# Kernel optimization log

Hardware: AMD Instinct MI355X
Metric: run time of the kernel (lower is better)

## Reference

```python
import jax, jax.numpy as jnp
import numpy as np

B, T, C, H = 2, 2048, 1024, 16
HD = C // H  # head dim = 64


def setup_inputs() -> dict:
    key = jax.random.key(0)
    k0, k1, k2 = jax.random.split(key, 3)
    x = jax.random.normal(k0, (B, T, C), jnp.float32)
    W_attn = jax.random.normal(k1, (C, 3 * C), jnp.float32) * 0.02
    b_attn = jnp.zeros((3 * C,), jnp.float32)
    W_proj = jax.random.normal(k2, (C, C), jnp.float32) * 0.02
    b_proj = jnp.zeros((C,), jnp.float32)
    # rope: (1,1,T,HD//2,2,2) stack of 2x2 rotation matrices [[cos,-sin],[sin,cos]]
    inv_freq = 1.0 / (10000.0 ** (jnp.arange(0, HD, 2, dtype=jnp.float32) / HD))
    ang = jnp.arange(T, dtype=jnp.float32)[:, None] * inv_freq[None, :]  # (T, HD//2)
    cos, sin = jnp.cos(ang), jnp.sin(ang)
    rope = jnp.stack([jnp.stack([cos, -sin], -1), jnp.stack([sin, cos], -1)], -2)
    rope = rope[None, None]  # (1,1,T,HD//2,2,2)
    return dict(x=x, W_attn=W_attn, b_attn=b_attn, W_proj=W_proj, b_proj=b_proj, rope=rope)


def reference(x, W_attn, b_attn, W_proj, b_proj, rope):
    Bv, Tv, Cv = x.shape
    Hd = Cv // H
    qkv = x @ W_attn + b_attn                      # (B,T,3C) fused QKV proj
    q, k, v = jnp.split(qkv, 3, axis=-1)

    def heads(t):
        return t.reshape(Bv, Tv, H, Hd).transpose(0, 2, 1, 3)  # (B,H,T,Hd)

    q, k, v = heads(q), heads(k), heads(v)

    cos = rope[..., 0, 0][..., None]               # (1,1,T,Hd//2,1)
    sin = rope[..., 1, 0][..., None]

    def rot(t):
        tr = t.reshape(Bv, H, Tv, Hd // 2, 2)
        xr, yr = tr[..., 0:1], tr[..., 1:2]
        out = jnp.concatenate([xr * cos - yr * sin, xr * sin + yr * cos], axis=-1)
        return out.reshape(Bv, H, Tv, Hd)

    q, k = rot(q), rot(k)

    scale = 1.0 / np.sqrt(Hd).astype(np.float32)
    att = jnp.einsum('bhqd,bhkd->bhqk', q, k) * scale
    mask = jnp.tril(jnp.ones((Tv, Tv), dtype=bool))  # causal
    att = jnp.where(mask[None, None], att, -jnp.inf)
    att = jax.nn.softmax(att, axis=-1)
    y = jnp.einsum('bhqk,bhkd->bhqd', att, v)
    y = y.transpose(0, 2, 1, 3).reshape(Bv, Tv, Cv)
    return y @ W_proj + b_proj
```

## Files before the change

### kernel.cpp

```cpp
#include <hip/hip_runtime.h>
#include <hip/hip_bf16.h>

typedef __attribute__((ext_vector_type(8))) short short8;
typedef __attribute__((ext_vector_type(4))) short short4b;
typedef __attribute__((ext_vector_type(4))) float f32x4;
typedef __attribute__((ext_vector_type(16))) float f32x16;
typedef __attribute__((ext_vector_type(4))) unsigned u32x4;

static constexpr int Bb = 2, Tt = 2048, Cc = 1024, Hh = 16;
static constexpr int BT = Bb * Tt;
static constexpr int N1 = 3 * Cc;
static constexpr float QS = 0.125f * 1.44269504f;

__device__ __forceinline__ unsigned short f2b(float f) {
  union { float f; unsigned u; } v; v.f = f;
  unsigned r = v.u + 0x7fffu + ((v.u >> 16) & 1u);
  return (unsigned short)(r >> 16);
}
__device__ __forceinline__ float b2f(short s) {
  union { unsigned u; float f; } v; v.u = ((unsigned)(unsigned short)s) << 16;
  return v.f;
}

__global__ __launch_bounds__(256) void k_cast(const float* __restrict__ in,
                                              unsigned short* __restrict__ out, int n) {
  int i = (blockIdx.x * 256 + threadIdx.x) * 8;
  if (i >= n) return;
  float4 a = *reinterpret_cast<const float4*>(in + i);
  float4 b = *reinterpret_cast<const float4*>(in + i + 4);
  short8 o;
  o[0] = f2b(a.x); o[1] = f2b(a.y); o[2] = f2b(a.z); o[3] = f2b(a.w);
  o[4] = f2b(b.x); o[5] = f2b(b.y); o[6] = f2b(b.z); o[7] = f2b(b.w);
  *reinterpret_cast<short8*>(out + i) = o;
}

__global__ __launch_bounds__(256) void k_tcast(const float* __restrict__ in,
                                               unsigned short* __restrict__ out,
                                               int R, int Ccol) {
  __shared__ float tile[32][33];
  int cb = blockIdx.x * 32, rb = blockIdx.y * 32;
  int tx = threadIdx.x & 31, ty = threadIdx.x >> 5;
  for (int i = 0; i < 32; i += 8)
    tile[ty + i][tx] = in[(size_t)(rb + ty + i) * Ccol + cb + tx];
  __syncthreads();
  for (int i = 0; i < 32; i += 8)
    out[(size_t)(cb + ty + i) * R + rb + tx] = f2b(tile[tx][ty + i]);
}

template <int BM, int NF, int EPI>
__global__ __launch_bounds__(512, 2)
void k_gemm8(const unsigned short* __restrict__ A, const unsigned short* __restrict__ Bt,
             const float* __restrict__ bias, void* __restrict__ Cout,
             const float* __restrict__ rope, unsigned short* __restrict__ Qs,
             unsigned short* __restrict__ Ks, unsigned short* __restrict__ Vt,
             int M, int N, int K) {
  constexpr int BN = NF * 64;
  constexpr int MF = BM / 32;
  constexpr int AI = BM / 64;
  constexpr int ASZ = BM * 64;
  constexpr int BSZ = BN * 64;
  constexpr int STRIDE = ASZ + BSZ;
  extern __shared__ unsigned short lds[];
  const int tid = threadIdx.x, lane = tid & 63, w = tid >> 6;
  const int wm = w >> 2, wn = w & 3;
  const int l15 = lane & 15, l4 = lane >> 4;
  int nbx = gridDim.x;
  int lin = blockIdx.y * nbx + blockIdx.x;
  int cpx = (nbx * gridDim.y) >> 3;
  lin = (lin & 7) * cpx + (lin >> 3);
  const int mb = lin / nbx, nb = lin % nbx;
  const size_t arow0 = (size_t)mb * BM;
  const size_t brow0 = (size_t)nb * BN;

  const int srow = lane >> 3;
  const int scol = (((lane & 7) * 16) ^ (srow << 4)) >> 1;
  auto stage = [&](int buf, int k0) {
    unsigned short* Ab = lds + buf * STRIDE;
    unsigned short* Bb = Ab + ASZ;
#pragma unroll
    for (int i = 0; i < AI; i++) {
      int c = w + 8 * i;
      const unsigned short* g = A + (arow0 + c * 8 + srow) * (size_t)K + k0 + scol;
      __builtin_amdgcn_global_load_lds((const __attribute__((address_space(1))) void*)g,
          (__attribute__((address_space(3))) void*)(Ab + c * 512), 16, 0, 0);
    }
#pragma unroll
    for (int i = 0; i < NF; i++) {
      int c = w + 8 * i;
      const unsigned short* g = Bt + (brow0 + c * 8 + srow) * (size_t)K + k0 + scol;
      __builtin_amdgcn_global_load_lds((const __attribute__((address_space(1))) void*)g,
          (__attribute__((address_space(3))) void*)(Bb + c * 512), 16, 0, 0);
    }
  };

  f32x4 acc[MF][NF] = {};
  const int NK = K >> 6;

  stage(0, 0);
  asm volatile("s_waitcnt vmcnt(0)" ::: "memory");
  asm volatile("s_barrier" ::: "memory");

  for (int kt = 0; kt < NK; kt++) {
    int buf = kt & 1;
    if (kt + 1 < NK) stage(buf ^ 1, (kt + 1) << 6);
    const unsigned short* Ab = lds + buf * STRIDE;
    const unsigned short* Bb = Ab + ASZ;
    short8 af[MF][2];
#pragma unroll
    for (int p = 0; p < NF; p++) {
      if (p == 0) {
#pragma unroll
        for (int m = 0; m < MF; m++) {
          int ra = wm * (BM / 2) + m * 16 + l15;
#pragma unroll
          for (int kk = 0; kk < 2; kk++) {
            int cb = (kk * 64 + l4 * 16) ^ ((ra & 7) << 4);
            af[m][kk] = *reinterpret_cast<const short8*>(Ab + ra * 64 + (cb >> 1));
          }
        }
      }
      short8 bfr[2];
      int rb = wn * (NF * 16) + p * 16 + l15;
#pragma unroll
      for (int kk = 0; kk < 2; kk++) {
        int cb = (kk * 64 + l4 * 16) ^ ((rb & 7) << 4);
        bfr[kk] = *reinterpret_cast<const short8*>(Bb + rb * 64 + (cb >> 1));
      }
      asm volatile("s_barrier" ::: "memory");
      asm volatile("s_waitcnt lgkmcnt(0)" ::: "memory");
      __builtin_amdgcn_sched_barrier(0);
      __builtin_amdgcn_s_setprio(1);
#pragma unroll
      for (int m = 0; m < MF; m++) {
        acc[m][p] = __builtin_amdgcn_mfma_f32_16x16x32_bf16(af[m][0], bfr[0], acc[m][p], 0, 0, 0);
        acc[m][p] = __builtin_amdgcn_mfma_f32_16x16x32_bf16(af[m][1], bfr[1], acc[m][p], 0, 0, 0);
      }
      __builtin_amdgcn_s_setprio(0);
      if (p == NF - 1)
        asm volatile("s_waitcnt vmcnt(0)" ::: "memory");
      asm volatile("s_barrier" ::: "memory");
    }
  }

#pragma unroll
  for (int m = 0; m < MF; m++) {
#pragma unroll
    for (int n = 0; n < NF; n++) {
      int ccol0 = nb * BN + wn * (NF * 16) + n * 16;
      float bv = bias[ccol0 + l15];
      int r0 = mb * BM + wm * (BM / 2) + m * 16 + l4 * 4;
      if (EPI == 0) {
#pragma unroll
        for (int j = 0; j < 4; j++)
          ((float*)Cout)[(size_t)(r0 + j) * N + ccol0 + l15] = acc[m][n][j] + bv;
      } else {
        int cls = ccol0 >> 10;
        int h = (ccol0 >> 6) & 15;
        int d = (ccol0 & 63) + l15;
        int bq = r0 >> 11;
        int t0 = r0 & 2047;
        size_t bh = (size_t)bq * 16 + h;
        if (cls == 2) {
          short4b o;
#pragma unroll
          for (int j = 0; j < 4; j++) o[j] = (short)f2b(acc[m][n][j] + bv);
          *reinterpret_cast<short4b*>(Vt + (bh * 64 + d) * Tt + t0) = o;
        } else {
          unsigned short* dst = (cls == 0) ? Qs : Ks;
          int jj = d >> 1;
          int odd = d & 1;
#pragma unroll
          for (int j = 0; j < 4; j++) {
            float v = acc[m][n][j] + bv;
            float part = __shfl_xor(v, 1);
            float2 sc = *reinterpret_cast<const float2*>(
                rope + (size_t)(t0 + j) * 128 + jj * 4 + 2);
            float x = odd ? part : v;
            float y = odd ? v : part;
            float rot = odd ? (x * sc.x + y * sc.y)
                            : (x * sc.y - y * sc.x);
            if (cls == 0) rot *= QS;
            dst[(bh * Tt + (t0 + j)) * 64 + d] = f2b(rot);
          }
        }
      }
    }
  }
}

__device__ __forceinline__ float tmax16(const f32x16& v) {
  float a0 = fmaxf(v[0], v[1]),   a1 = fmaxf(v[2], v[3]);
  float a2 = fmaxf(v[4], v[5]),   a3 = fmaxf(v[6], v[7]);
  float a4 = fmaxf(v[8], v[9]),   a5 = fmaxf(v[10], v[11]);
  float a6 = fmaxf(v[12], v[13]), a7 = fmaxf(v[14], v[15]);
  float b0 = fmaxf(a0, a1), b1 = fmaxf(a2, a3), b2 = fmaxf(a4, a5), b3 = fmaxf(a6, a7);
  return fmaxf(fmaxf(b0, b1), fmaxf(b2, b3));
}

__device__ __forceinline__ void attn_tile64(
    const unsigned short* Kl, const unsigned short* Vl,
    int w, int l31, int hi, const short8 qf[4],
    float& m_run, float& l_run, f32x16 oacc[2], int grelBase) {
  f32x16 sc[2];
  bool act[2];
#pragma unroll
  for (int kt = 0; kt < 2; kt++) {
    int grel = grelBase + kt;
    act[kt] = (grel <= w);
    if (!act[kt]) continue;
    f32x16 acc = {};
    int rk = kt * 32 + l31;
    int sw = (rk & 7) << 4;
    const unsigned short* krow = Kl + rk * 64;
    short8 kf[4];
#pragma unroll
    for (int kk = 0; kk < 4; kk++)
      kf[kk] = *reinterpret_cast<const short8*>(krow + (((kk * 32 + hi * 16) ^ sw) >> 1));
    __builtin_amdgcn_s_setprio(1);
#pragma unroll
    for (int kk = 0; kk < 4; kk++)
      acc = __builtin_amdgcn_mfma_f32_32x32x16_bf16(kf[kk], qf[kk], acc, 0, 0, 0);
    __builtin_amdgcn_s_setprio(0);
    if (grel == w) {
#pragma unroll
      for (int r = 0; r < 16; r++) {
        int e = (r & 3) + 8 * (r >> 2) + 4 * hi;
        if (e > l31) acc[r] = -1e30f;
      }
    }
    sc[kt] = acc;
  }
  float km0 = act[0] ? tmax16(sc[0]) : -1e30f;
  float km1 = act[1] ? tmax16(sc[1]) : -1e30f;
  float mx = fmaxf(km0, km1);
  mx = fmaxf(mx, __shfl_xor(mx, 32));

  float fsc = 1.f;
  if (!__all(mx <= m_run + 8.f)) {
    float nm = fmaxf(m_run, mx);
    fsc = __builtin_amdgcn_exp2f(m_run - nm);
    m_run = nm;
#pragma unroll
    for (int dt = 0; dt < 2; dt++)
#pragma unroll
      for (int r = 0; r < 16; r++) oacc[dt][r] *= fsc;
  }

  float kps[2] = {0.f, 0.f};
#pragma unroll
  for (int kt = 0; kt < 2; kt++) {
    if (!act[kt]) continue;
    float p[16];
#pragma unroll
    for (int r = 0; r < 16; r++) p[r] = __builtin_amdgcn_exp2f(sc[kt][r] - m_run);
    float s0 = (p[0] + p[1]) + (p[2] + p[3]);
    float s1 = (p[4] + p[5]) + (p[6] + p[7]);
    float s2 = (p[8] + p[9]) + (p[10] + p[11]);
    float s3 = (p[12] + p[13]) + (p[14] + p[15]);
    kps[kt] = (s0 + s1) + (s2 + s3);
    unsigned P[8];
#pragma unroll
    for (int i = 0; i < 8; i++)
      asm("v_cvt_pk_bf16_f32 %0, %1, %2" : "=v"(P[i]) : "v"(p[2 * i]), "v"(p[2 * i + 1]));
    unsigned Y0 = (unsigned)__shfl_xor((int)(hi ? P[0] : P[2]), 32);
    unsigned Y1 = (unsigned)__shfl_xor((int)(hi ? P[1] : P[3]), 32);
    unsigned Y2 = (unsigned)__shfl_xor((int)(hi ? P[4] : P[6]), 32);
    unsigned Y3 = (unsigned)__shfl_xor((int)(hi ? P[5] : P[7]), 32);
    u32x4 c0 = hi ? u32x4{Y0, Y1, P[2], P[3]} : u32x4{P[0], P[1], Y0, Y1};
    u32x4 c1 = hi ? u32x4{Y2, Y3, P[6], P[7]} : u32x4{P[4], P[5], Y2, Y3};
    short8 pf0 = __builtin_bit_cast(short8, c0);
    short8 pf1 = __builtin_bit_cast(short8, c1);
#pragma unroll
    for (int dt = 0; dt < 2; dt++) {
      int d = dt * 32 + l31;
      int sv = (d & 7) << 4;
      const unsigned short* vrow = Vl + d * 64;
      short8 vf0 = *reinterpret_cast<const short8*>(vrow + (((kt * 64 + hi * 16) ^ sv) >> 1));
      short8 vf1 = *reinterpret_cast<const short8*>(vrow + (((kt * 64 + 32 + hi * 16) ^ sv) >> 1));
      __builtin_amdgcn_s_setprio(1);
      oacc[dt] = __builtin_amdgcn_mfma_f32_32x32x16_bf16(vf0, pf0, oacc[dt], 0, 0, 0);
      oacc[dt] = __builtin_amdgcn_mfma_f32_32x32x16_bf16(vf1, pf1, oacc[dt], 0, 0, 0);
      __builtin_amdgcn_s_setprio(0);
    }
  }
  float psum = kps[0] + kps[1];
  psum += __shfl_xor(psum, 32);
  l_run = l_run * fsc + psum;
}

__global__ __launch_bounds__(256)
void k_attn1(const unsigned short* __restrict__ Qs, const unsigned short* __restrict__ Ks,
             const unsigned short* __restrict__ Vt, unsigned short* __restrict__ Opart,
             float* __restrict__ ml) {
  __shared__ unsigned short lds[16384];
  int tid = threadIdx.x, lane = tid & 63, w = tid >> 6;
  int sid = blockIdx.x;
  int qb = 15 - (sid >> 6);
  int c = (sid >> 5) & 1;
  int bh = sid & 31;
  int l31 = lane & 31, hi = lane >> 5;
  int qw0 = qb * 128 + w * 32;
  const unsigned short* Qb = Qs + (size_t)bh * Tt * 64;
  const unsigned short* Kb = Ks + (size_t)bh * Tt * 64;
  const unsigned short* Vb = Vt + (size_t)bh * 64 * Tt;

  const int NT = 2 * qb + 2;
  const int half = NT >> 1;
  const int t0 = c ? half : 0;
  const int t1 = c ? NT : half;

  auto stage = [&](int buf, int kv0) {
    unsigned short* Kbuf = lds + buf * 4096;
    unsigned short* Vbuf = lds + 8192 + buf * 4096;
    int r8 = lane >> 3;
    int colb = ((lane & 7) * 16) ^ (r8 << 4);
#pragma unroll
    for (int cc = 0; cc < 2; cc++) {
      int ch = w + cc * 4;
      const unsigned short* gk = Kb + (size_t)(kv0 + ch * 8 + r8) * 64 + (colb >> 1);
      __builtin_amdgcn_global_load_lds((const __attribute__((address_space(1))) void*)gk,
          (__attribute__((address_space(3))) void*)(Kbuf + ch * 512), 16, 0, 0);
      const unsigned short* gv = Vb + (size_t)(ch * 8 + r8) * Tt + kv0 + (colb >> 1);
      __builtin_amdgcn_global_load_lds((const __attribute__((address_space(1))) void*)gv,
          (__attribute__((address_space(3))) void*)(Vbuf + ch * 512), 16, 0, 0);
    }
  };

  short8 qf[4];
#pragma unroll
  for (int kk = 0; kk < 4; kk++)
    qf[kk] = *reinterpret_cast<const short8*>(Qb + (size_t)(qw0 + l31) * 64 + kk * 16 + hi * 8);

  float m_run = -1e30f, l_run = 0.f;
  f32x16 oacc[2] = {};

  stage(0, t0 * 64);
  __syncthreads();
  int cur = 0;
  for (int T = t0; T < t1; ++T) {
    if (T + 1 < t1) stage(cur ^ 1, (T + 1) * 64);
    attn_tile64(lds + cur * 4096, lds + 8192 + cur * 4096,
                w, l31, hi, qf, m_run, l_run, oacc, 2 * T - 4 * qb);
    __syncthreads();
    cur ^= 1;
  }

  size_t orow = (size_t)sid * 128 + w * 32 + l31;
#pragma unroll
  for (int dt = 0; dt < 2; dt++)
#pragma unroll
    for (int q4 = 0; q4 < 4; q4++) {
      short4b oo;
#pragma unroll
      for (int jj = 0; jj < 4; jj++) oo[jj] = (short)f2b(oacc[dt][q4 * 4 + jj]);
      *reinterpret_cast<short4b*>(Opart + orow * 64 + dt * 32 + q4 * 8 + hi * 4) = oo;
    }
  if (hi == 0) {
    float2 v; v.x = m_run; v.y = l_run;
    *reinterpret_cast<float2*>(ml + orow * 2) = v;
  }
}

__global__ __launch_bounds__(256)
void k_attn2(const unsigned short* __restrict__ Opart, const float* __restrict__ ml,
             unsigned short* __restrict__ Y) {
  int gid = blockIdx.x * 256 + threadIdx.x;
  int row = gid >> 3;
  int dblk = (gid & 7) * 8;
  int bh = row >> 11, q = row & 2047;
  int qb = q >> 7, qrow = q & 127;
  int s0 = (15 - qb) * 64 + bh;
  int s1 = s0 + 32;
  float2 ml0 = *reinterpret_cast<const float2*>(ml + ((size_t)s0 * 128 + qrow) * 2);
  float2 ml1 = *reinterpret_cast<const float2*>(ml + ((size_t)s1 * 128 + qrow) * 2);
  float m = fmaxf(ml0.x, ml1.x);
  float w0 = __builtin_amdgcn_exp2f(ml0.x - m);
  float w1 = __builtin_amdgcn_exp2f(ml1.x - m);
  float inv = 1.0f / (w0 * ml0.y + w1 * ml1.y);
  float a0 = w0 * inv, a1 = w1 * inv;
  short8 o0 = *reinterpret_cast<const short8*>(Opart + ((size_t)s0 * 128 + qrow) * 64 + dblk);
  short8 o1 = *reinterpret_cast<const short8*>(Opart + ((size_t)s1 * 128 + qrow) * 64 + dblk);
  short8 o;
#pragma unroll
  for (int j = 0; j < 8; j++) o[j] = (short)f2b(b2f(o0[j]) * a0 + b2f(o1[j]) * a1);
  int b = bh >> 4, h = bh & 15;
  *reinterpret_cast<short8*>(Y + ((size_t)(b * Tt + q)) * Cc + h * 64 + dblk) = o;
}

extern "C" void kernel_launch(void* const* d_in, const int* in_sizes, int n_in,
                              void* d_out, int out_size, void* d_ws, size_t ws_size,
                              hipStream_t stream) {
  (void)in_sizes; (void)n_in; (void)out_size; (void)ws_size;
  const float* x      = (const float*)d_in[0];
  const float* W_attn = (const float*)d_in[1];
  const float* b_attn = (const float*)d_in[2];
  const float* W_proj = (const float*)d_in[3];
  const float* b_proj = (const float*)d_in[4];
  const float* rope   = (const float*)d_in[5];
  float* out = (float*)d_out;

  char* ws = (char*)d_ws;
  unsigned short* xb    = (unsigned short*)(ws);
  unsigned short* WaT   = (unsigned short*)(ws + (8u << 20));
  unsigned short* WpT   = (unsigned short*)(ws + (14u << 20));
  unsigned short* Qs    = (unsigned short*)(ws + (16u << 20));
  unsigned short* Ks    = (unsigned short*)(ws + (24u << 20));
  unsigned short* Vt    = (unsigned short*)(ws + (32u << 20));
  unsigned short* Yb    = (unsigned short*)(ws + (40u << 20));
  unsigned short* Opart = (unsigned short*)(ws + (48u << 20));
  float*          ml    = (float*)(ws + (64u << 20));

  constexpr int LDS_QKV  = (128 + 192) * 64 * 2 * 2;
  constexpr int LDS_PROJ = (128 + 128) * 64 * 2 * 2;
  (void)hipFuncSetAttribute(reinterpret_cast<const void*>(&k_gemm8<128, 3, 1>),
                            hipFuncAttributeMaxDynamicSharedMemorySize, LDS_QKV);
  (void)hipFuncSetAttribute(reinterpret_cast<const void*>(&k_gemm8<128, 2, 0>),
                            hipFuncAttributeMaxDynamicSharedMemorySize, LDS_PROJ);

  k_cast<<<2048, 256, 0, stream>>>(x, xb, BT * Cc);
  k_tcast<<<dim3(N1 / 32, Cc / 32), 256, 0, stream>>>(W_attn, WaT, Cc, N1);
  k_tcast<<<dim3(Cc / 32, Cc / 32), 256, 0, stream>>>(W_proj, WpT, Cc, Cc);
  k_gemm8<128, 3, 1><<<dim3(N1 / 192, BT / 128), 512, LDS_QKV, stream>>>(
      xb, WaT, b_attn, nullptr, rope, Qs, Ks, Vt, BT, N1, Cc);
  k_attn1<<<1024, 256, 0, stream>>>(Qs, Ks, Vt, Opart, ml);
  k_attn2<<<2048, 256, 0, stream>>>(Opart, ml, Yb);
  k_gemm8<128, 2, 0><<<dim3(Cc / 128, BT / 128), 512, LDS_PROJ, stream>>>(
      Yb, WpT, b_proj, out, nullptr, nullptr, nullptr, nullptr, BT, Cc, Cc);
}
```

Baseline: 107.6 us.

## Triple-buffer K/V staging in attention with manual vmcnt waits and diagonal-specialized tiles

The attention kernel moves from double to triple buffering of K/V tiles in LDS. Loads are prefetched two tiles ahead, and the full __syncthreads is replaced by explicit s_waitcnt vmcnt plus s_barrier, so one tile's load can still be in flight at the barrier. Tile processing is templated on the buffer slot and on whether it is a diagonal tile, which removes mask checks from off-diagonal tiles and precomputes the swizzled LDS offsets once. The row-sum cross-lane shuffle is deferred to the end of the kernel. In exchange the kernel uses more LDS, which may lower occupancy, and the hand-written vmcnt counts depend on the exact number of load instructions issued per stage.

```diff
diff --git a/kernel.cpp b/kernel.cpp
--- a/kernel.cpp
+++ b/kernel.cpp
@@ -197,44 +197,42 @@
   return fmaxf(fmaxf(b0, b1), fmaxf(b2, b3));
 }
 
-__device__ __forceinline__ void attn_tile64(
-    const unsigned short* Kl, const unsigned short* Vl,
+template <int SLOT, bool DIAG>
+__device__ __forceinline__ void tile64(
+    const unsigned short* ldsp, const unsigned off_k[4], const unsigned off_v[4],
     int w, int l31, int hi, const short8 qf[4],
     float& m_run, float& l_run, f32x16 oacc[2], int grelBase) {
+  constexpr int KB = SLOT * 8192;
+  constexpr int VB = KB + 4096;
   f32x16 sc[2];
-  bool act[2];
+  const bool act0 = !DIAG || (grelBase <= w);
+  const bool act1 = !DIAG || (grelBase + 1 <= w);
 #pragma unroll
   for (int kt = 0; kt < 2; kt++) {
-    int grel = grelBase + kt;
-    act[kt] = (grel <= w);
-    if (!act[kt]) continue;
-    f32x16 acc = {};
-    int rk = kt * 32 + l31;
-    int sw = (rk & 7) << 4;
-    const unsigned short* krow = Kl + rk * 64;
+    if (DIAG && !(kt == 0 ? act0 : act1)) continue;
+    f32x16 a = {};
     short8 kf[4];
 #pragma unroll
     for (int kk = 0; kk < 4; kk++)
-      kf[kk] = *reinterpret_cast<const short8*>(krow + (((kk * 32 + hi * 16) ^ sw) >> 1));
+      kf[kk] = *reinterpret_cast<const short8*>(ldsp + KB + kt * 2048 + off_k[kk]);
     __builtin_amdgcn_s_setprio(1);
 #pragma unroll
     for (int kk = 0; kk < 4; kk++)
-      acc = __builtin_amdgcn_mfma_f32_32x32x16_bf16(kf[kk], qf[kk], acc, 0, 0, 0);
+      a = __builtin_amdgcn_mfma_f32_32x32x16_bf16(kf[kk], qf[kk], a, 0, 0, 0);
     __builtin_amdgcn_s_setprio(0);
-    if (grel == w) {
+    if (DIAG && grelBase + kt == w) {
 #pragma unroll
       for (int r = 0; r < 16; r++) {
         int e = (r & 3) + 8 * (r >> 2) + 4 * hi;
-        if (e > l31) acc[r] = -1e30f;
+        if (e > l31) a[r] = -1e30f;
       }
     }
-    sc[kt] = acc;
-  }
-  float km0 = act[0] ? tmax16(sc[0]) : -1e30f;
-  float km1 = act[1] ? tmax16(sc[1]) : -1e30f;
+    sc[kt] = a;
+  }
+  float km0 = act0 ? tmax16(sc[0]) : -1e30f;
+  float km1 = act1 ? tmax16(sc[1]) : -1e30f;
   float mx = fmaxf(km0, km1);
   mx = fmaxf(mx, __shfl_xor(mx, 32));
-
   float fsc = 1.f;
   if (!__all(mx <= m_run + 8.f)) {
     float nm = fmaxf(m_run, mx);
@@ -245,11 +243,10 @@
 #pragma unroll
       for (int r = 0; r < 16; r++) oacc[dt][r] *= fsc;
   }
-
-  float kps[2] = {0.f, 0.f};
+  l_run *= fsc;
 #pragma unroll
   for (int kt = 0; kt < 2; kt++) {
-    if (!act[kt]) continue;
+    if (DIAG && !(kt == 0 ? act0 : act1)) continue;
     float p[16];
 #pragma unroll
     for (int r = 0; r < 16; r++) p[r] = __builtin_amdgcn_exp2f(sc[kt][r] - m_run);
@@ -257,7 +254,7 @@
     float s1 = (p[4] + p[5]) + (p[6] + p[7]);
     float s2 = (p[8] + p[9]) + (p[10] + p[11]);
     float s3 = (p[12] + p[13]) + (p[14] + p[15]);
-    kps[kt] = (s0 + s1) + (s2 + s3);
+    l_run += (s0 + s1) + (s2 + s3);
     unsigned P[8];
 #pragma unroll
     for (int i = 0; i < 8; i++)
@@ -272,27 +269,21 @@
     short8 pf1 = __builtin_bit_cast(short8, c1);
 #pragma unroll
     for (int dt = 0; dt < 2; dt++) {
-      int d = dt * 32 + l31;
-      int sv = (d & 7) << 4;
-      const unsigned short* vrow = Vl + d * 64;
-      short8 vf0 = *reinterpret_cast<const short8*>(vrow + (((kt * 64 + hi * 16) ^ sv) >> 1));
-      short8 vf1 = *reinterpret_cast<const short8*>(vrow + (((kt * 64 + 32 + hi * 16) ^ sv) >> 1));
+      short8 vf0 = *reinterpret_cast<const short8*>(ldsp + VB + dt * 2048 + off_v[kt * 2]);
+      short8 vf1 = *reinterpret_cast<const short8*>(ldsp + VB + dt * 2048 + off_v[kt * 2 + 1]);
       __builtin_amdgcn_s_setprio(1);
       oacc[dt] = __builtin_amdgcn_mfma_f32_32x32x16_bf16(vf0, pf0, oacc[dt], 0, 0, 0);
       oacc[dt] = __builtin_amdgcn_mfma_f32_32x32x16_bf16(vf1, pf1, oacc[dt], 0, 0, 0);
       __builtin_amdgcn_s_setprio(0);
     }
   }
-  float psum = kps[0] + kps[1];
-  psum += __shfl_xor(psum, 32);
-  l_run = l_run * fsc + psum;
 }
 
 __global__ __launch_bounds__(256)
 void k_attn1(const unsigned short* __restrict__ Qs, const unsigned short* __restrict__ Ks,
              const unsigned short* __restrict__ Vt, unsigned short* __restrict__ Opart,
              float* __restrict__ ml) {
-  __shared__ unsigned short lds[16384];
+  __shared__ unsigned short lds[24576];
   int tid = threadIdx.x, lane = tid & 63, w = tid >> 6;
   int sid = blockIdx.x;
   int qb = 15 - (sid >> 6);
@@ -304,46 +295,84 @@
   const unsigned short* Kb = Ks + (size_t)bh * Tt * 64;
   const unsigned short* Vb = Vt + (size_t)bh * 64 * Tt;
 
-  const int NT = 2 * qb + 2;
-  const int half = NT >> 1;
-  const int t0 = c ? half : 0;
-  const int t1 = c ? NT : half;
-
-  auto stage = [&](int buf, int kv0) {
-    unsigned short* Kbuf = lds + buf * 4096;
-    unsigned short* Vbuf = lds + 8192 + buf * 4096;
-    int r8 = lane >> 3;
-    int colb = ((lane & 7) * 16) ^ (r8 << 4);
-#pragma unroll
-    for (int cc = 0; cc < 2; cc++) {
-      int ch = w + cc * 4;
-      const unsigned short* gk = Kb + (size_t)(kv0 + ch * 8 + r8) * 64 + (colb >> 1);
-      __builtin_amdgcn_global_load_lds((const __attribute__((address_space(1))) void*)gk,
-          (__attribute__((address_space(3))) void*)(Kbuf + ch * 512), 16, 0, 0);
-      const unsigned short* gv = Vb + (size_t)(ch * 8 + r8) * Tt + kv0 + (colb >> 1);
-      __builtin_amdgcn_global_load_lds((const __attribute__((address_space(1))) void*)gv,
-          (__attribute__((address_space(3))) void*)(Vbuf + ch * 512), 16, 0, 0);
-    }
-  };
-
   short8 qf[4];
 #pragma unroll
   for (int kk = 0; kk < 4; kk++)
     qf[kk] = *reinterpret_cast<const short8*>(Qb + (size_t)(qw0 + l31) * 64 + kk * 16 + hi * 8);
 
+  const int sw = (l31 & 7) << 4;
+  unsigned off_k[4], off_v[4];
+#pragma unroll
+  for (int kk = 0; kk < 4; kk++)
+    off_k[kk] = (unsigned)(l31 * 128 + ((kk * 32 + hi * 16) ^ sw)) >> 1;
+#pragma unroll
+  for (int i = 0; i < 4; i++)
+    off_v[i] = (unsigned)(l31 * 128 + (((i >> 1) * 64 + (i & 1) * 32 + hi * 16) ^ sw)) >> 1;
+
+  const int r8 = lane >> 3;
+  const int colb = ((lane & 7) * 16) ^ (r8 << 4);
+  const unsigned short* gK0 = Kb + (size_t)(w * 8 + r8) * 64 + (colb >> 1);
+  const unsigned short* gV0 = Vb + (size_t)(w * 8 + r8) * Tt + (colb >> 1);
+
+  auto stage = [&](int slot, int T) {
+    unsigned short* sb = lds + slot * 8192;
+    const unsigned short* k0 = gK0 + (size_t)T * 4096;
+    const unsigned short* v0 = gV0 + (size_t)T * 64;
+    __builtin_amdgcn_global_load_lds((const __attribute__((address_space(1))) void*)k0,
+        (__attribute__((address_space(3))) void*)(sb + w * 512), 16, 0, 0);
+    __builtin_amdgcn_global_load_lds((const __attribute__((address_space(1))) void*)(k0 + 2048),
+        (__attribute__((address_space(3))) void*)(sb + (w + 4) * 512), 16, 0, 0);
+    __builtin_amdgcn_global_load_lds((const __attribute__((address_space(1))) void*)v0,
+        (__attribute__((address_space(3))) void*)(sb + 4096 + w * 512), 16, 0, 0);
+    __builtin_amdgcn_global_load_lds((const __attribute__((address_space(1))) void*)(v0 + (size_t)32 * Tt),
+        (__attribute__((address_space(3))) void*)(sb + 4096 + (w + 4) * 512), 16, 0, 0);
+  };
+
+  const int NT = 2 * qb + 2, half = NT >> 1;
+  const int t0 = c ? half : 0, t1 = c ? NT : half;
+  const int diagT = 2 * qb;
+
   float m_run = -1e30f, l_run = 0.f;
   f32x16 oacc[2] = {};
 
-  stage(0, t0 * 64);
-  __syncthreads();
-  int cur = 0;
+  stage(0, t0);
+  if (t0 + 1 < t1) {
+    stage(1, t0 + 1);
+    asm volatile("s_waitcnt vmcnt(4)" ::: "memory");
+  } else {
+    asm volatile("s_waitcnt vmcnt(0)" ::: "memory");
+  }
+  asm volatile("s_barrier" ::: "memory");
+
+  int sl = 0;
   for (int T = t0; T < t1; ++T) {
-    if (T + 1 < t1) stage(cur ^ 1, (T + 1) * 64);
-    attn_tile64(lds + cur * 4096, lds + 8192 + cur * 4096,
-                w, l31, hi, qf, m_run, l_run, oacc, 2 * T - 4 * qb);
-    __syncthreads();
-    cur ^= 1;
-  }
+    bool more2 = (T + 2 < t1);
+    if (more2) stage(sl == 0 ? 2 : sl - 1, T + 2);
+    int gB = 2 * T - 4 * qb;
+    bool full = T < diagT;
+    switch (sl) {
+      case 0:
+        if (full) tile64<0, false>(lds, off_k, off_v, w, l31, hi, qf, m_run, l_run, oacc, 0);
+        else      tile64<0, true >(lds, off_k, off_v, w, l31, hi, qf, m_run, l_run, oacc, gB);
+        break;
+      case 1:
+        if (full) tile64<1, false>(lds, off_k, off_v, w, l31, hi, qf, m_run, l_run, oacc, 0);
+        else      tile64<1, true >(lds, off_k, off_v, w, l31, hi, qf, m_run, l_run, oacc, gB);
+        break;
+      default:
+        if (full) tile64<2, false>(lds, off_k, off_v, w, l31, hi, qf, m_run, l_run, oacc, 0);
+        else      tile64<2, true >(lds, off_k, off_v, w, l31, hi, qf, m_run, l_run, oacc, gB);
+        break;
+    }
+    if (T + 1 < t1) {
+      if (more2) asm volatile("s_waitcnt vmcnt(4)" ::: "memory");
+      else       asm volatile("s_waitcnt vmcnt(0)" ::: "memory");
+      asm volatile("s_barrier" ::: "memory");
+    }
+    sl = (sl == 2) ? 0 : sl + 1;
+  }
+
+  l_run += __shfl_xor(l_run, 32);
 
   size_t orow = (size_t)sid * 128 + w * 32 + l31;
 #pragma unroll
```

Result: no change. 109.5 us (+1.8%).
